# Kernel optimization log

Measured on AMD Instinct MI355X. Metric: run time of the kernel, lower is better.

The kernel has to match this reference:

```python
import jax, jax.numpy as jnp
import numpy as np
from jax import lax

B, T, QD, ED, AD = 256, 512, 1024, 512, 128
NF, KS = 32, 31  # location filters, kernel size
PAD = (KS - 1) // 2


def setup_inputs() -> dict:
    key = jax.random.key(0)
    ks = jax.random.split(key, 12)
    query = jax.random.normal(ks[0], (B, QD), jnp.float32)
    inputs = jax.random.normal(ks[1], (B, T, ED), jnp.float32)
    processed_inputs = jax.random.normal(ks[2], (B, T, AD), jnp.float32)
    mask = jnp.ones((B, T), jnp.bool_)
    # init_states()
    attention_weights = jnp.zeros((B, T), jnp.float32)
    attention_weights_cum = jnp.zeros((B, T), jnp.float32)
    alpha = jnp.concatenate([jnp.ones((B, 1)), jnp.full((B, T - 1), 1e-7)], axis=1).astype(jnp.float32)
    u = 0.5 * jnp.ones((B, 1), jnp.float32)
    # parameters (xavier-ish scale)
    Wq = jax.random.normal(ks[3], (QD, AD), jnp.float32) * 0.03
    conv_w = jax.random.normal(ks[4], (NF, 2, KS), jnp.float32) * 0.1  # OIH
    Wloc = jax.random.normal(ks[5], (NF, AD), jnp.float32) * 0.1
    v_w = jax.random.normal(ks[6], (AD, 1), jnp.float32) * 0.1
    v_b = jnp.zeros((1,), jnp.float32)
    ta_w = jax.random.normal(ks[7], (ED + QD, 1), jnp.float32) * 0.02
    ta_b = jnp.zeros((1,), jnp.float32)
    return dict(query=query, inputs=inputs, processed_inputs=processed_inputs, mask=mask,
                attention_weights=attention_weights, attention_weights_cum=attention_weights_cum,
                alpha=alpha, u=u, Wq=Wq, conv_w=conv_w, Wloc=Wloc, v_w=v_w, v_b=v_b,
                ta_w=ta_w, ta_b=ta_b)


def reference(query, inputs, processed_inputs, mask, attention_weights,
              attention_weights_cum, alpha, u, Wq, conv_w, Wloc, v_w, v_b, ta_w, ta_b):
    # location-sensitive energies
    att_cat = jnp.stack([attention_weights, attention_weights_cum], axis=1)  # [B,2,T]
    loc = lax.conv_general_dilated(att_cat, conv_w, (1,), [(PAD, PAD)],
                                   dimension_numbers=('NCH', 'OIH', 'NCH'))  # [B,NF,T]
    proc_attn = jnp.einsum('bft,fa->bta', loc, Wloc)                         # [B,T,AD]
    proc_query = (query @ Wq)[:, None, :]                                    # [B,1,AD]
    energies = (jnp.tanh(proc_query + proc_attn + processed_inputs) @ v_w + v_b)[..., 0]  # [B,T]
    energies = jnp.where(mask, energies, -jnp.inf)
    alignment = jax.nn.softmax(energies, axis=-1)
    # forward attention recursion (training mode, no forward_attn_mask)
    shifted = jnp.pad(alpha[:, :-1], ((0, 0), (1, 0)))
    alpha_new = ((1.0 - u) * alpha + u * shifted + 1e-8) * alignment
    alpha_new = alpha_new / jnp.sum(alpha_new, axis=1, keepdims=True)
    context = jnp.einsum('bt,btd->bd', alpha_new, inputs)                    # [B,ED]
    # transition agent (state update; computed for faithfulness)
    u_new = jax.nn.sigmoid(jnp.concatenate([context, query], axis=-1) @ ta_w + ta_b)
    del u_new
    return context
```

## Files before the change

### kernel.cpp

```cpp
#include <hip/hip_runtime.h>

#define BB 256
#define TT 512
#define QD 1024
#define ED 512
#define AD 128
#define NF 32
#define KS 31
#define PADL 15
#define TCHUNK 256
#define NSEG 16

typedef float f32x4 __attribute__((ext_vector_type(4)));

__device__ __forceinline__ float tanh_fast(float x) {
    float ex = __expf(2.0f * x);
    return 1.0f - 2.0f / (ex + 1.0f);
}

__global__ __launch_bounds__(256) void k_pq(const float* __restrict__ query,
                                            const float* __restrict__ Wq,
                                            float* __restrict__ pq) {
    int b = blockIdx.x;
    int tid = threadIdx.x;
    __shared__ float qs[QD];
    __shared__ float part[256];
    for (int i = tid; i < QD; i += 256) qs[i] = query[(size_t)b * QD + i];
    __syncthreads();
    int half = tid >> 7;
    int a = tid & 127;
    int kbase = half * 512;
    const float* wp = Wq + (size_t)kbase * AD + a;
    float acc = 0.f;
#pragma unroll 8
    for (int k = 0; k < 512; ++k)
        acc = fmaf(qs[kbase + k], wp[(size_t)k * AD], acc);
    part[tid] = acc;
    __syncthreads();
    if (tid < 128) pq[(size_t)b * AD + tid] = part[tid] + part[tid + 128];
}

__global__ __launch_bounds__(256) void k_energies(
    const float* __restrict__ attW, const float* __restrict__ attC,
    const float* __restrict__ convw, const float* __restrict__ Wloc,
    const float* __restrict__ pq, const float* __restrict__ pin,
    const float* __restrict__ vw, const float* __restrict__ vb,
    float* __restrict__ energies) {
    int b = blockIdx.x;
    int t0 = blockIdx.y * TCHUNK;
    int tid = threadIdx.x;

    __shared__ float sA[TCHUNK + 2 * PADL];
    __shared__ float sC[TCHUNK + 2 * PADL];
    __shared__ float sLoc[TCHUNK * 36];

    for (int i = tid; i < TCHUNK + 2 * PADL; i += 256) {
        int t = t0 + i - PADL;
        float a = 0.f, c = 0.f;
        if (t >= 0 && t < TT) {
            a = attW[(size_t)b * TT + t];
            c = attC[(size_t)b * TT + t];
        }
        sA[i] = a;
        sC[i] = c;
    }
    __syncthreads();

    {
        float winA[KS], winC[KS];
#pragma unroll
        for (int k = 0; k < KS; ++k) {
            winA[k] = sA[tid + k];
            winC[k] = sC[tid + k];
        }
        float* lrow = sLoc + tid * 36;
        for (int f = 0; f < NF; ++f) {
            const float* cwa = convw + f * (2 * KS);
            float acc = 0.f;
#pragma unroll
            for (int k = 0; k < KS; ++k) {
                acc = fmaf(cwa[k], winA[k], acc);
                acc = fmaf(cwa[KS + k], winC[k], acc);
            }
            lrow[f] = acc;
        }
    }
    __syncthreads();

    int wid = tid >> 6, lane = tid & 63;
    float2 w2[NF];
#pragma unroll
    for (int f = 0; f < NF; ++f)
        w2[f] = ((const float2*)(Wloc + f * AD))[lane];
    float2 pq2 = ((const float2*)(pq + (size_t)b * AD))[lane];
    float2 vw2 = ((const float2*)vw)[lane];
    float vbv = vb[0];

    for (int tt = wid; tt < TCHUNK; tt += 4) {
        int t = t0 + tt;
        const float4* lr = (const float4*)(sLoc + tt * 36);
        float pa0 = 0.f, pa1 = 0.f;
#pragma unroll
        for (int j = 0; j < 8; ++j) {
            float4 Lv = lr[j];
            pa0 = fmaf(Lv.x, w2[4 * j + 0].x, pa0);
            pa1 = fmaf(Lv.x, w2[4 * j + 0].y, pa1);
            pa0 = fmaf(Lv.y, w2[4 * j + 1].x, pa0);
            pa1 = fmaf(Lv.y, w2[4 * j + 1].y, pa1);
            pa0 = fmaf(Lv.z, w2[4 * j + 2].x, pa0);
            pa1 = fmaf(Lv.z, w2[4 * j + 2].y, pa1);
            pa0 = fmaf(Lv.w, w2[4 * j + 3].x, pa0);
            pa1 = fmaf(Lv.w, w2[4 * j + 3].y, pa1);
        }
        float2 p2 = ((const float2*)pin)[(size_t)(b * TT + t) * (AD / 2) + lane];
        float x0 = pq2.x + pa0 + p2.x;
        float x1 = pq2.y + pa1 + p2.y;
        float e = tanh_fast(x0) * vw2.x + tanh_fast(x1) * vw2.y;
#pragma unroll
        for (int off = 32; off > 0; off >>= 1)
            e += __shfl_xor(e, off, 64);
        if (lane == 0) energies[(size_t)b * TT + t] = e + vbv;
    }
}

__global__ __launch_bounds__(256) void k_alpha(
    const float* __restrict__ energies, const float* __restrict__ alpha,
    const float* __restrict__ uArr, float* __restrict__ alphaN) {
    int b = blockIdx.x, tid = threadIdx.x;
    int lane = tid & 63, wid = tid >> 6;
    size_t base = (size_t)b * TT;
    float e0 = energies[base + tid];
    float e1 = energies[base + tid + 256];
    float m = fmaxf(e0, e1);
#pragma unroll
    for (int off = 32; off > 0; off >>= 1) m = fmaxf(m, __shfl_xor(m, off, 64));
    __shared__ float redm[4];
    __shared__ float reds[4];
    if (lane == 0) redm[wid] = m;
    __syncthreads();
    m = fmaxf(fmaxf(redm[0], redm[1]), fmaxf(redm[2], redm[3]));

    float u = uArr[b];
    float a0 = alpha[base + tid];
    float a1 = alpha[base + tid + 256];
    float ap0 = (tid == 0) ? 0.f : alpha[base + tid - 1];
    float ap1 = alpha[base + tid + 255];
    float p0 = __expf(e0 - m), p1 = __expf(e1 - m);
    float q0 = fmaf(1.f - u, a0, u * ap0 + 1e-8f) * p0;
    float q1 = fmaf(1.f - u, a1, u * ap1 + 1e-8f) * p1;
    float s = q0 + q1;
#pragma unroll
    for (int off = 32; off > 0; off >>= 1) s += __shfl_xor(s, off, 64);
    if (lane == 0) reds[wid] = s;
    __syncthreads();
    s = (reds[0] + reds[1]) + (reds[2] + reds[3]);
    float inv = 1.f / s;
    alphaN[base + tid] = q0 * inv;
    alphaN[base + tid + 256] = q1 * inv;
}

__global__ __launch_bounds__(128) void k_ctx_partial(
    const float* __restrict__ alphaN, const float* __restrict__ inputs,
    float* __restrict__ partial) {
    int b = blockIdx.x, s = blockIdx.y, tid = threadIdx.x;
    const int tlen = TT / NSEG;
    int t0 = s * tlen;
    __shared__ float al[tlen];
    if (tid < tlen) al[tid] = alphaN[(size_t)b * TT + t0 + tid];
    __syncthreads();
    const f32x4* in4 = (const f32x4*)inputs;
    size_t base = ((size_t)b * TT + t0) * (ED / 4) + tid;
    f32x4 acc = (f32x4)(0.f);
#pragma unroll 8
    for (int j = 0; j < tlen; ++j) {
        f32x4 v = __builtin_nontemporal_load(&in4[base + (size_t)j * (ED / 4)]);
        float w = al[j];
        acc.x = fmaf(w, v.x, acc.x);
        acc.y = fmaf(w, v.y, acc.y);
        acc.z = fmaf(w, v.z, acc.z);
        acc.w = fmaf(w, v.w, acc.w);
    }
    ((f32x4*)partial)[((size_t)(b * NSEG + s)) * (ED / 4) + tid] = acc;
}

__global__ __launch_bounds__(256) void k_ctx_reduce(
    const float* __restrict__ partial, float* __restrict__ out) {
    int idx = blockIdx.x * 256 + threadIdx.x;
    int b = idx >> 7, d4 = idx & 127;
    const f32x4* p4 = (const f32x4*)partial;
    f32x4 s = (f32x4)(0.f);
#pragma unroll
    for (int j = 0; j < NSEG; ++j) {
        f32x4 v = p4[((size_t)(b * NSEG + j)) * (ED / 4) + d4];
        s += v;
    }
    ((f32x4*)out)[idx] = s;
}

extern "C" void kernel_launch(void* const* d_in, const int* in_sizes, int n_in,
                              void* d_out, int out_size, void* d_ws, size_t ws_size,
                              hipStream_t stream) {
    (void)in_sizes; (void)n_in; (void)out_size; (void)ws_size;
    const float* query = (const float*)d_in[0];
    const float* inputs = (const float*)d_in[1];
    const float* pin   = (const float*)d_in[2];
    const float* attW  = (const float*)d_in[4];
    const float* attC  = (const float*)d_in[5];
    const float* alpha = (const float*)d_in[6];
    const float* uArr  = (const float*)d_in[7];
    const float* Wq    = (const float*)d_in[8];
    const float* convw = (const float*)d_in[9];
    const float* Wloc  = (const float*)d_in[10];
    const float* vw    = (const float*)d_in[11];
    const float* vb    = (const float*)d_in[12];

    float* ws = (float*)d_ws;
    float* pq       = ws;
    float* energies = pq + BB * AD;
    float* alphaN   = energies + BB * TT;
    float* partial  = alphaN + BB * TT;

    k_pq<<<dim3(BB), dim3(256), 0, stream>>>(query, Wq, pq);
    k_energies<<<dim3(BB, TT / TCHUNK), dim3(256), 0, stream>>>(
        attW, attC, convw, Wloc, pq, pin, vw, vb, energies);
    k_alpha<<<dim3(BB), dim3(256), 0, stream>>>(energies, alpha, uArr, alphaN);
    k_ctx_partial<<<dim3(BB, NSEG), dim3(128), 0, stream>>>(alphaN, inputs, partial);
    k_ctx_reduce<<<dim3((BB * ED / 4) / 256), dim3(256), 0, stream>>>(partial, (float*)d_out);
}
```

Before: 133.1 us.

## Fuse softmax-alpha, context partial sums and reduction into one kernel

Merges the alpha normalisation, the segmented context accumulation and the final reduction into a single 1024-thread block per batch row. Alpha stays in shared memory and the eight partial accumulators are reduced in LDS, so the alphaN and partial workspace round trips and two kernel launches go away. In exchange the bandwidth-heavy context read now runs on only 256 large blocks instead of thousands of small ones, which may reduce memory-level parallelism.

```diff
diff --git a/kernel.cpp b/kernel.cpp
--- a/kernel.cpp
+++ b/kernel.cpp
@@ -9,7 +9,6 @@
 #define KS 31
 #define PADL 15
 #define TCHUNK 256
-#define NSEG 16
 
 typedef float f32x4 __attribute__((ext_vector_type(4)));
 
@@ -123,78 +122,72 @@
     }
 }
 
-__global__ __launch_bounds__(256) void k_alpha(
+__global__ __launch_bounds__(1024) void k_alpha_ctx(
     const float* __restrict__ energies, const float* __restrict__ alpha,
-    const float* __restrict__ uArr, float* __restrict__ alphaN) {
-    int b = blockIdx.x, tid = threadIdx.x;
+    const float* __restrict__ uArr, const float* __restrict__ inputs,
+    float* __restrict__ out) {
+    int b = blockIdx.x;
+    int tid = threadIdx.x;
     int lane = tid & 63, wid = tid >> 6;
+
+    __shared__ float al[TT];
+    __shared__ float red[16];
+    __shared__ f32x4 sacc[8][128];
+
     size_t base = (size_t)b * TT;
-    float e0 = energies[base + tid];
-    float e1 = energies[base + tid + 256];
-    float m = fmaxf(e0, e1);
+    float e = -1e30f, a0 = 0.f, ap = 0.f;
+    if (tid < TT) {
+        e = energies[base + tid];
+        a0 = alpha[base + tid];
+        ap = (tid == 0) ? 0.f : alpha[base + tid - 1];
+    }
+    float m = e;
 #pragma unroll
     for (int off = 32; off > 0; off >>= 1) m = fmaxf(m, __shfl_xor(m, off, 64));
-    __shared__ float redm[4];
-    __shared__ float reds[4];
-    if (lane == 0) redm[wid] = m;
-    __syncthreads();
-    m = fmaxf(fmaxf(redm[0], redm[1]), fmaxf(redm[2], redm[3]));
+    if (lane == 0) red[wid] = m;
+    __syncthreads();
+    m = red[0];
+#pragma unroll
+    for (int i = 1; i < 16; ++i) m = fmaxf(m, red[i]);
 
     float u = uArr[b];
-    float a0 = alpha[base + tid];
-    float a1 = alpha[base + tid + 256];
-    float ap0 = (tid == 0) ? 0.f : alpha[base + tid - 1];
-    float ap1 = alpha[base + tid + 255];
-    float p0 = __expf(e0 - m), p1 = __expf(e1 - m);
-    float q0 = fmaf(1.f - u, a0, u * ap0 + 1e-8f) * p0;
-    float q1 = fmaf(1.f - u, a1, u * ap1 + 1e-8f) * p1;
-    float s = q0 + q1;
+    float q = 0.f;
+    if (tid < TT)
+        q = fmaf(1.f - u, a0, u * ap + 1e-8f) * __expf(e - m);
+    float s = q;
 #pragma unroll
     for (int off = 32; off > 0; off >>= 1) s += __shfl_xor(s, off, 64);
-    if (lane == 0) reds[wid] = s;
-    __syncthreads();
-    s = (reds[0] + reds[1]) + (reds[2] + reds[3]);
-    float inv = 1.f / s;
-    alphaN[base + tid] = q0 * inv;
-    alphaN[base + tid + 256] = q1 * inv;
-}
-
-__global__ __launch_bounds__(128) void k_ctx_partial(
-    const float* __restrict__ alphaN, const float* __restrict__ inputs,
-    float* __restrict__ partial) {
-    int b = blockIdx.x, s = blockIdx.y, tid = threadIdx.x;
-    const int tlen = TT / NSEG;
-    int t0 = s * tlen;
-    __shared__ float al[tlen];
-    if (tid < tlen) al[tid] = alphaN[(size_t)b * TT + t0 + tid];
-    __syncthreads();
+    __syncthreads();
+    if (lane == 0) red[wid] = s;
+    __syncthreads();
+    s = 0.f;
+#pragma unroll
+    for (int i = 0; i < 16; ++i) s += red[i];
+    if (tid < TT) al[tid] = q / s;
+    __syncthreads();
+
+    int g = tid >> 7;
+    int c = tid & 127;
     const f32x4* in4 = (const f32x4*)inputs;
-    size_t base = ((size_t)b * TT + t0) * (ED / 4) + tid;
+    size_t rb = ((size_t)b * TT + (size_t)g * 64) * (ED / 4) + c;
     f32x4 acc = (f32x4)(0.f);
 #pragma unroll 8
-    for (int j = 0; j < tlen; ++j) {
-        f32x4 v = __builtin_nontemporal_load(&in4[base + (size_t)j * (ED / 4)]);
-        float w = al[j];
+    for (int j = 0; j < 64; ++j) {
+        f32x4 v = __builtin_nontemporal_load(&in4[rb + (size_t)j * (ED / 4)]);
+        float w = al[g * 64 + j];
         acc.x = fmaf(w, v.x, acc.x);
         acc.y = fmaf(w, v.y, acc.y);
         acc.z = fmaf(w, v.z, acc.z);
         acc.w = fmaf(w, v.w, acc.w);
     }
-    ((f32x4*)partial)[((size_t)(b * NSEG + s)) * (ED / 4) + tid] = acc;
-}
-
-__global__ __launch_bounds__(256) void k_ctx_reduce(
-    const float* __restrict__ partial, float* __restrict__ out) {
-    int idx = blockIdx.x * 256 + threadIdx.x;
-    int b = idx >> 7, d4 = idx & 127;
-    const f32x4* p4 = (const f32x4*)partial;
-    f32x4 s = (f32x4)(0.f);
-#pragma unroll
-    for (int j = 0; j < NSEG; ++j) {
-        f32x4 v = p4[((size_t)(b * NSEG + j)) * (ED / 4) + d4];
-        s += v;
-    }
-    ((f32x4*)out)[idx] = s;
+    sacc[g][c] = acc;
+    __syncthreads();
+    if (tid < 128) {
+        f32x4 t = sacc[0][tid];
+#pragma unroll
+        for (int i = 1; i < 8; ++i) t += sacc[i][tid];
+        ((f32x4*)out)[(size_t)b * (ED / 4) + tid] = t;
+    }
 }
 
 extern "C" void kernel_launch(void* const* d_in, const int* in_sizes, int n_in,
@@ -217,13 +210,10 @@
     float* ws = (float*)d_ws;
     float* pq       = ws;
     float* energies = pq + BB * AD;
-    float* alphaN   = energies + BB * TT;
-    float* partial  = alphaN + BB * TT;
 
     k_pq<<<dim3(BB), dim3(256), 0, stream>>>(query, Wq, pq);
     k_energies<<<dim3(BB, TT / TCHUNK), dim3(256), 0, stream>>>(
         attW, attC, convw, Wloc, pq, pin, vw, vb, energies);
-    k_alpha<<<dim3(BB), dim3(256), 0, stream>>>(energies, alpha, uArr, alphaN);
-    k_ctx_partial<<<dim3(BB, NSEG), dim3(128), 0, stream>>>(alphaN, inputs, partial);
-    k_ctx_reduce<<<dim3((BB * ED / 4) / 256), dim3(256), 0, stream>>>(partial, (float*)d_out);
-}
+    k_alpha_ctx<<<dim3(BB), dim3(1024), 0, stream>>>(
+        energies, alpha, uArr, inputs, (float*)d_out);
+}
```

Result: faster. 124.5 us (-6.4%).
